# Performance work log

Measured on AMD Instinct MI355X. Metric: run time of the kernel, lower is better.

Reference implementation:

```python
import jax, jax.numpy as jnp
import numpy as np

N_NODES = 100000
N_EDGES = 3200000
IN_DIM = 512
OUT_DIM = 128


def setup_inputs() -> dict:
    key = jax.random.key(0)
    kx, kw, kr, kc, kv = jax.random.split(key, 5)
    x = jax.random.normal(kx, (N_NODES, IN_DIM), dtype=jnp.float32)
    # glorot uniform init for the weight, matching glorot_init in the source
    init_range = np.sqrt(6.0 / (IN_DIM + OUT_DIM)).astype(np.float32)
    W = jax.random.uniform(kw, (IN_DIM, OUT_DIM), dtype=jnp.float32,
                           minval=-init_range, maxval=init_range)
    edge_row = jax.random.randint(kr, (N_EDGES,), 0, N_NODES, dtype=jnp.int32)
    edge_col = jax.random.randint(kc, (N_EDGES,), 0, N_NODES, dtype=jnp.int32)
    edge_val = jax.random.uniform(kv, (N_EDGES,), dtype=jnp.float32)
    return {"x": x, "W": W, "edge_row": edge_row, "edge_col": edge_col,
            "edge_val": edge_val}


def reference(x, W, edge_row, edge_col, edge_val):
    # dense projection: [N, in] @ [in, out] -> [N, out]
    xp = x @ W
    # SpMM: out[r] += val * xp[c] for each edge (r, c, val)
    msgs = xp[edge_col] * edge_val[:, None]          # [E, out]
    agg = jax.ops.segment_sum(msgs, edge_row, num_segments=N_NODES)
    return jax.nn.relu(agg)
```

## Files before the change

kernel.cpp:

```cpp
#include <hip/hip_runtime.h>

#define M_NODES 100000
#define MPAD    100096
#define K_DIM   512
#define N_DIM   128
#define NUM_EDGES 3200000

#define RSHIFT  6
#define ROWS_PB 64
#define NBUCK   1563
#define BCAP    2432
#define EPW     4096
#define NAPPEND ((NUM_EDGES + EPW - 1) / EPW)
#define GEMM_BLOCKS (MPAD / 128)

#define BK      32
#define KSTEPS  (K_DIM / BK)

typedef __bf16 bf16x8 __attribute__((ext_vector_type(8)));
typedef float f32x16 __attribute__((ext_vector_type(16)));
typedef unsigned short ushort8 __attribute__((ext_vector_type(8)));
typedef unsigned int uint32;

typedef __attribute__((address_space(1))) const unsigned int gas_u32;
typedef __attribute__((address_space(3))) unsigned int las_u32;

__device__ __forceinline__ unsigned short f2bf(float f) {
  uint32 u = __float_as_uint(f);
  u = (u + 0x7FFFu + ((u >> 16) & 1u)) >> 16;
  return (unsigned short)u;
}

__device__ __forceinline__ float bf_lo(uint32 m) {
  return __uint_as_float(m << 16);
}
__device__ __forceinline__ float bf_hi(uint32 m) {
  return __uint_as_float(m & 0xFFFF0000u);
}

__global__ __launch_bounds__(256) void wfrag_kernel(
    const float* __restrict__ W, unsigned short* __restrict__ Wf,
    int* __restrict__ gcursor) {
  const int t = blockIdx.x * 256 + threadIdx.x;
  const int j = t & 7;
  const int lane = (t >> 3) & 63;
  const int ng = (t >> 9) & 3;
  const int ks = t >> 11;
  const int k = ks * 16 + ((lane >> 5) << 3) + j;
  const int n = (ng << 5) + (lane & 31);
  Wf[t] = f2bf(W[k * N_DIM + n]);
  if (t < NBUCK) gcursor[t] = 0;
}

__device__ __forceinline__ void stage_tile(float* dst,
                                           const float* __restrict__ x,
                                           int row0, int k0, int w, int lane) {
#pragma unroll
  for (int i = 0; i < 4; ++i) {
    const int seg = i * 4 + w;
    const int d = seg * 1024 + lane * 16;
    const int row = d >> 7;
    const int ch = (d >> 4) & 7;
    const int sch = ch ^ (row & 7);
    int gr = row0 + row;
    if (gr >= M_NODES) gr = M_NODES - 1;
    const float* src = x + (size_t)gr * K_DIM + k0 + sch * 4;
    __builtin_amdgcn_global_load_lds((gas_u32*)src,
                                     (las_u32*)(dst + seg * 256), 16, 0, 0);
  }
}

__device__ __forceinline__ bf16x8 read_a_frag(const float* As, int r, int ks,
                                              int hi) {
  const int c0 = ks * 4 + hi * 2;
  const int sw = r & 7;
  const float4 f0 = *(const float4*)(As + r * 32 + ((c0 ^ sw) << 2));
  const float4 f1 = *(const float4*)(As + r * 32 + (((c0 + 1) ^ sw) << 2));
  ushort8 u;
  u[0] = f2bf(f0.x); u[1] = f2bf(f0.y); u[2] = f2bf(f0.z); u[3] = f2bf(f0.w);
  u[4] = f2bf(f1.x); u[5] = f2bf(f1.y); u[6] = f2bf(f1.z); u[7] = f2bf(f1.w);
  return __builtin_bit_cast(bf16x8, u);
}

__device__ __forceinline__ void gemm_body(int bx, char* smem,
                                          const float* __restrict__ x,
                                          const unsigned short* __restrict__ Wf,
                                          unsigned short* __restrict__ xp) {
  float* A0 = (float*)smem;
  float* A1 = (float*)(smem + 16384);

  const int tid = threadIdx.x;
  const int w = tid >> 6;
  const int lane = tid & 63;
  const int l31 = lane & 31;
  const int lhi = lane >> 5;
  const int row0 = bx * 128;
  const int r = w * 32 + l31;

  f32x16 acc[4] = {};

  stage_tile(A0, x, row0, 0, w, lane);
  __syncthreads();

  for (int t = 0; t < KSTEPS; ++t) {
    float* cur = (t & 1) ? A1 : A0;
    float* nxt = (t & 1) ? A0 : A1;
    if (t + 1 < KSTEPS) stage_tile(nxt, x, row0, (t + 1) * BK, w, lane);

    const int ksg0 = t * 2;
#pragma unroll
    for (int ks = 0; ks < 2; ++ks) {
      const bf16x8 a = read_a_frag(cur, r, ks, lhi);
      const ushort8* bp =
          (const ushort8*)(Wf) + ((size_t)(ksg0 + ks) * 4 * 64 + lane);
#pragma unroll
      for (int ng = 0; ng < 4; ++ng) {
        const bf16x8 b = __builtin_bit_cast(bf16x8, bp[(size_t)ng * 64]);
        acc[ng] =
            __builtin_amdgcn_mfma_f32_32x32x16_bf16(a, b, acc[ng], 0, 0, 0);
      }
    }
    __syncthreads();
  }

  const int rbase = row0 + w * 32 + 4 * lhi;
#pragma unroll
  for (int ng = 0; ng < 4; ++ng) {
    const int cc = (ng << 5) + l31;
#pragma unroll
    for (int reg = 0; reg < 16; ++reg) {
      const int rr = rbase + (reg & 3) + 8 * (reg >> 2);
      xp[(size_t)rr * N_DIM + cc] = f2bf(acc[ng][reg]);
    }
  }
}

__device__ __forceinline__ int tag_edge(int r, int* lcnt) {
  const int b = r >> RSHIFT;
  const int s = atomicAdd(&lcnt[b], 1);
  return (b << 18) | (s << 6) | (r & (ROWS_PB - 1));
}

__device__ __forceinline__ void emit_edge(int p, int col, float v,
                                          const int* lbase,
                                          uint2* __restrict__ buckets) {
  const int b = (int)((unsigned)p >> 18);
  const int idx = lbase[b] + ((p >> 6) & 0xFFF);
  if (idx < BCAP)
    buckets[(size_t)b * BCAP + idx] = make_uint2(
        ((uint32)col << 6) | (uint32)(p & (ROWS_PB - 1)), __float_as_uint(v));
}

__device__ __forceinline__ void bin_body(int bx, char* smem,
                                         const int* __restrict__ erow,
                                         const int* __restrict__ ecol,
                                         const float* __restrict__ eval,
                                         int* __restrict__ gcursor,
                                         uint2* __restrict__ buckets) {
  int* lcnt = (int*)smem;
  int* lbase = (int*)(smem + 6912);
  const int tid = threadIdx.x;
  for (int i = tid; i < NBUCK; i += 256) lcnt[i] = 0;
  __syncthreads();

  const int base = bx * EPW;
  int pk[16];
#pragma unroll
  for (int c = 0; c < 4; ++c) {
    const int e0 = base + c * 1024 + tid * 4;
    if (e0 < NUM_EDGES) {
      const int4 r4 = *(const int4*)(erow + e0);
      pk[c * 4 + 0] = tag_edge(r4.x, lcnt);
      pk[c * 4 + 1] = tag_edge(r4.y, lcnt);
      pk[c * 4 + 2] = tag_edge(r4.z, lcnt);
      pk[c * 4 + 3] = tag_edge(r4.w, lcnt);
    }
  }
  __syncthreads();

  for (int i = tid; i < NBUCK; i += 256) {
    const int c = lcnt[i];
    lbase[i] = c ? atomicAdd(&gcursor[i], c) : 0;
  }
  __syncthreads();

#pragma unroll
  for (int c = 0; c < 4; ++c) {
    const int e0 = base + c * 1024 + tid * 4;
    if (e0 < NUM_EDGES) {
      const int4 c4 = *(const int4*)(ecol + e0);
      const float4 v4 = *(const float4*)(eval + e0);
      emit_edge(pk[c * 4 + 0], c4.x, v4.x, lbase, buckets);
      emit_edge(pk[c * 4 + 1], c4.y, v4.y, lbase, buckets);
      emit_edge(pk[c * 4 + 2], c4.z, v4.z, lbase, buckets);
      emit_edge(pk[c * 4 + 3], c4.w, v4.w, lbase, buckets);
    }
  }
}

__global__ __launch_bounds__(256) void gemm_bin_kernel(
    const float* __restrict__ x, const unsigned short* __restrict__ Wf,
    unsigned short* __restrict__ xp, const int* __restrict__ erow,
    const int* __restrict__ ecol, const float* __restrict__ eval,
    int* __restrict__ gcursor, uint2* __restrict__ buckets) {
  __shared__ __align__(16) char smem[32768];
  if (blockIdx.x < GEMM_BLOCKS) {
    gemm_body(blockIdx.x, smem, x, Wf, xp);
  } else {
    bin_body(blockIdx.x - GEMM_BLOCKS, smem, erow, ecol, eval, gcursor,
             buckets);
  }
}

__global__ __launch_bounds__(256, 8) void bucket_gather_kernel(
    const unsigned short* __restrict__ xp, const int* __restrict__ gcursor,
    const uint2* __restrict__ buckets, float* __restrict__ out) {
  __shared__ uint2 eds[BCAP];
  __shared__ int rbase[ROWS_PB + 1];
  __shared__ int rcur[ROWS_PB];
  __shared__ int stmp[ROWS_PB];

  const int b = blockIdx.x;
  const int tid = threadIdx.x;
  int n = gcursor[b];
  if (n > BCAP) n = BCAP;

  if (tid < ROWS_PB) rcur[tid] = 0;
  __syncthreads();

  const uint2* bk = buckets + (size_t)b * BCAP;
  for (int i = tid; i < n; i += 256) atomicAdd(&rcur[bk[i].x & 63], 1);
  __syncthreads();

  if (tid < ROWS_PB) stmp[tid] = rcur[tid];
  __syncthreads();
  for (int off = 1; off < ROWS_PB; off <<= 1) {
    int v = 0, a = 0;
    if (tid < ROWS_PB) {
      v = stmp[tid];
      if (tid >= off) a = stmp[tid - off];
    }
    __syncthreads();
    if (tid < ROWS_PB) stmp[tid] = v + a;
    __syncthreads();
  }
  if (tid < ROWS_PB) {
    rbase[tid + 1] = stmp[tid];
    rcur[tid] = 0;
  }
  if (tid == 0) rbase[0] = 0;
  __syncthreads();

  for (int i = tid; i < n; i += 256) {
    const uint2 e = bk[i];
    const int rl = e.x & 63;
    const int pos = rbase[rl] + atomicAdd(&rcur[rl], 1);
    eds[pos] = e;
  }
  __syncthreads();

  const int wv = tid >> 6;
  const int lane = tid & 63;
  const uint32* xpl = (const uint32*)xp + lane;

  for (int rl = wv; rl < ROWS_PB; rl += 4) {
    const int row = (b << RSHIFT) + rl;
    if (row >= M_NODES) break;
    const int s = rbase[rl];
    const int e = rbase[rl + 1];

    float ax0 = 0.f, ay0 = 0.f, ax1 = 0.f, ay1 = 0.f;
    float ax2 = 0.f, ay2 = 0.f, ax3 = 0.f, ay3 = 0.f;
    int i = s;
    for (; i + 3 < e; i += 4) {
      const uint2 e0 = eds[i];
      const uint2 e1 = eds[i + 1];
      const uint2 e2 = eds[i + 2];
      const uint2 e3 = eds[i + 3];
      const uint32 m0 = xpl[(size_t)(e0.x >> 6) * 64];
      const uint32 m1 = xpl[(size_t)(e1.x >> 6) * 64];
      const uint32 m2 = xpl[(size_t)(e2.x >> 6) * 64];
      const uint32 m3 = xpl[(size_t)(e3.x >> 6) * 64];
      const float v0 = __uint_as_float(e0.y);
      const float v1 = __uint_as_float(e1.y);
      const float v2 = __uint_as_float(e2.y);
      const float v3 = __uint_as_float(e3.y);
      ax0 += v0 * bf_lo(m0); ay0 += v0 * bf_hi(m0);
      ax1 += v1 * bf_lo(m1); ay1 += v1 * bf_hi(m1);
      ax2 += v2 * bf_lo(m2); ay2 += v2 * bf_hi(m2);
      ax3 += v3 * bf_lo(m3); ay3 += v3 * bf_hi(m3);
    }
    for (; i < e; ++i) {
      const uint2 e0 = eds[i];
      const uint32 m0 = xpl[(size_t)(e0.x >> 6) * 64];
      const float v0 = __uint_as_float(e0.y);
      ax0 += v0 * bf_lo(m0);
      ay0 += v0 * bf_hi(m0);
    }

    float2 r;
    r.x = fmaxf((ax0 + ax1) + (ax2 + ax3), 0.f);
    r.y = fmaxf((ay0 + ay1) + (ay2 + ay3), 0.f);
    *(float2*)(out + (size_t)row * N_DIM + lane * 2) = r;
  }
}

extern "C" void kernel_launch(void* const* d_in, const int* in_sizes, int n_in,
                              void* d_out, int out_size, void* d_ws,
                              size_t ws_size, hipStream_t stream) {
  const float* x = (const float*)d_in[0];
  const float* W = (const float*)d_in[1];
  const int* erow = (const int*)d_in[2];
  const int* ecol = (const int*)d_in[3];
  const float* eval = (const float*)d_in[4];
  float* out = (float*)d_out;

  char* wsb = (char*)d_ws;
  size_t off = 0;
  auto alloc = [&](size_t bytes) {
    char* p = wsb + off;
    off = (off + bytes + 511) & ~(size_t)511;
    return p;
  };
  unsigned short* xp =
      (unsigned short*)alloc((size_t)MPAD * N_DIM * sizeof(unsigned short));
  unsigned short* Wf =
      (unsigned short*)alloc((size_t)K_DIM * N_DIM * sizeof(unsigned short));
  int* gcursor = (int*)alloc((size_t)NBUCK * sizeof(int));
  uint2* buckets = (uint2*)alloc((size_t)NBUCK * BCAP * sizeof(uint2));
  (void)ws_size;

  wfrag_kernel<<<(K_DIM * N_DIM) / 256, 256, 0, stream>>>(W, Wf, gcursor);

  gemm_bin_kernel<<<GEMM_BLOCKS + NAPPEND, 256, 0, stream>>>(
      x, Wf, xp, erow, ecol, eval, gcursor, buckets);

  bucket_gather_kernel<<<NBUCK, 256, 0, stream>>>(xp, gcursor, buckets, out);
}
```

Before: 487.7 us.

## Stage W fragments into LDS alongside A tiles with explicit vmcnt waits

The GEMM now double-buffers the pre-fragmented bf16 weight tile in LDS together with the x tile, using async global_load_lds, instead of reading W fragments straight from global memory for each MFMA. The __syncthreads calls become manual s_waitcnt vmcnt plus s_barrier, so the next tile's loads can stay in flight while the current tile is computed. LDS per block grows from 32KB to 48KB, which may lower occupancy for both the GEMM and the binning blocks that share this kernel. The hand-written vmcnt counts must match the number of outstanding loads exactly, or the code reads stale data.

```diff
diff --git a/kernel.cpp b/kernel.cpp
--- a/kernel.cpp
+++ b/kernel.cpp
@@ -16,6 +16,9 @@
 
 #define BK      32
 #define KSTEPS  (K_DIM / BK)
+#define ABYTES  16384
+#define WBYTES  8192
+#define BUFBYTES (ABYTES + WBYTES)
 
 typedef __bf16 bf16x8 __attribute__((ext_vector_type(8)));
 typedef float f32x16 __attribute__((ext_vector_type(16)));
@@ -52,9 +55,9 @@
   if (t < NBUCK) gcursor[t] = 0;
 }
 
-__device__ __forceinline__ void stage_tile(float* dst,
-                                           const float* __restrict__ x,
-                                           int row0, int k0, int w, int lane) {
+__device__ __forceinline__ void stage_a(float* dst,
+                                        const float* __restrict__ x,
+                                        int row0, int k0, int w, int lane) {
 #pragma unroll
   for (int i = 0; i < 4; ++i) {
     const int seg = i * 4 + w;
@@ -70,6 +73,19 @@
   }
 }
 
+__device__ __forceinline__ void stage_w(unsigned short* dst,
+                                        const unsigned short* __restrict__ Wf,
+                                        int t, int w, int lane) {
+#pragma unroll
+  for (int i = 0; i < 2; ++i) {
+    const int seg = i * 4 + w;
+    const unsigned short* src =
+        Wf + (size_t)t * 4096 + seg * 512 + lane * 8;
+    __builtin_amdgcn_global_load_lds((gas_u32*)src,
+                                     (las_u32*)(dst + seg * 512), 16, 0, 0);
+  }
+}
+
 __device__ __forceinline__ bf16x8 read_a_frag(const float* As, int r, int ks,
                                               int hi) {
   const int c0 = ks * 4 + hi * 2;
@@ -87,7 +103,9 @@
                                           const unsigned short* __restrict__ Wf,
                                           unsigned short* __restrict__ xp) {
   float* A0 = (float*)smem;
-  float* A1 = (float*)(smem + 16384);
+  unsigned short* W0 = (unsigned short*)(smem + ABYTES);
+  float* A1 = (float*)(smem + BUFBYTES);
+  unsigned short* W1 = (unsigned short*)(smem + BUFBYTES + ABYTES);
 
   const int tid = threadIdx.x;
   const int w = tid >> 6;
@@ -99,20 +117,27 @@
 
   f32x16 acc[4] = {};
 
-  stage_tile(A0, x, row0, 0, w, lane);
-  __syncthreads();
+  stage_a(A0, x, row0, 0, w, lane);
+  stage_w(W0, Wf, 0, w, lane);
 
   for (int t = 0; t < KSTEPS; ++t) {
-    float* cur = (t & 1) ? A1 : A0;
-    float* nxt = (t & 1) ? A0 : A1;
-    if (t + 1 < KSTEPS) stage_tile(nxt, x, row0, (t + 1) * BK, w, lane);
-
-    const int ksg0 = t * 2;
+    float* Ac = (t & 1) ? A1 : A0;
+    unsigned short* Wc = (t & 1) ? W1 : W0;
+    if (t + 1 < KSTEPS) {
+      float* An = (t & 1) ? A0 : A1;
+      unsigned short* Wn = (t & 1) ? W0 : W1;
+      stage_a(An, x, row0, (t + 1) * BK, w, lane);
+      stage_w(Wn, Wf, t + 1, w, lane);
+      asm volatile("s_waitcnt vmcnt(6)" ::: "memory");
+    } else {
+      asm volatile("s_waitcnt vmcnt(0)" ::: "memory");
+    }
+    __builtin_amdgcn_s_barrier();
+
 #pragma unroll
     for (int ks = 0; ks < 2; ++ks) {
-      const bf16x8 a = read_a_frag(cur, r, ks, lhi);
-      const ushort8* bp =
-          (const ushort8*)(Wf) + ((size_t)(ksg0 + ks) * 4 * 64 + lane);
+      const bf16x8 a = read_a_frag(Ac, r, ks, lhi);
+      const ushort8* bp = (const ushort8*)Wc + (size_t)ks * 4 * 64 + lane;
 #pragma unroll
       for (int ng = 0; ng < 4; ++ng) {
         const bf16x8 b = __builtin_bit_cast(bf16x8, bp[(size_t)ng * 64]);
@@ -120,7 +145,7 @@
             __builtin_amdgcn_mfma_f32_32x32x16_bf16(a, b, acc[ng], 0, 0, 0);
       }
     }
-    __syncthreads();
+    __builtin_amdgcn_s_barrier();
   }
 
   const int rbase = row0 + w * 32 + 4 * lhi;
@@ -203,7 +228,7 @@
     unsigned short* __restrict__ xp, const int* __restrict__ erow,
     const int* __restrict__ ecol, const float* __restrict__ eval,
     int* __restrict__ gcursor, uint2* __restrict__ buckets) {
-  __shared__ __align__(16) char smem[32768];
+  __shared__ __align__(16) char smem[2 * BUFBYTES];
   if (blockIdx.x < GEMM_BLOCKS) {
     gemm_body(blockIdx.x, smem, x, Wf, xp);
   } else {
```

After: 474.1 us. 2.8% less time.
